# Kernel optimization log

Measured on AMD Instinct MI355X. Metric: run time of the kernel, lower is better.

## Reference

```python
import jax, jax.numpy as jnp
import numpy as np


def setup_inputs() -> dict:
    key = jax.random.key(0)
    k1, k2 = jax.random.split(key)
    B, D, T_ENC, T_DEC = 16, 256, 512, 2048
    x = jax.random.normal(k1, (B, D, T_ENC), dtype=jnp.float32)
    path = jax.random.uniform(k2, (B, T_ENC, T_DEC), dtype=jnp.float32)
    return {"x": x, "path": path}


def reference(x, path):
    # Batched matmul: [B, D, T_enc] @ [B, T_enc, T_dec] -> [B, D, T_dec]
    return jnp.einsum('bde,bet->bdt', x, path)
```

## Files before the change

kernel.cpp:

```cpp
#include <hip/hip_runtime.h>
#include <hip/hip_bf16.h>

#define NB 16
#define ND 256
#define NK 512
#define NT 2048

#define BM 128
#define BN 128
#define BK 32
#define RSA 40
#define RSB 36

typedef __attribute__((ext_vector_type(8))) short short8;
typedef __attribute__((ext_vector_type(4))) float f32x4;

union S8U { short8 v; uint2 u[2]; };
union BF2U { __hip_bfloat162 h; unsigned int u; };

__device__ inline unsigned int pack2bf(float a, float b) {
    BF2U c; c.h = __float22bfloat162_rn(make_float2(a, b));
    return c.u;
}

__global__ __launch_bounds__(256, 2)
void bmm_bf16_mfma(const float* __restrict__ x, const float* __restrict__ path,
                   float* __restrict__ out) {
    const int n0 = blockIdx.x * BN;
    const int m0 = blockIdx.y * BM;
    const int b  = blockIdx.z;
    const int t    = threadIdx.x;
    const int lane = t & 63;
    const int wv   = t >> 6;
    const int wr   = (wv >> 1) * 64;
    const int wc   = (wv & 1) * 64;
    const int q    = lane >> 4;
    const int lm   = lane & 15;

    __shared__ unsigned short As[BM * RSA];
    __shared__ unsigned short Bs[BN * RSB];

    const float* xg = x    + ((size_t)b * ND + m0) * NK;
    const float* pg = path + (size_t)b * NK * NT + n0;

    f32x4 acc[4][4];
#pragma unroll
    for (int i = 0; i < 4; ++i)
#pragma unroll
        for (int j = 0; j < 4; ++j)
            acc[i][j] = (f32x4){0.f, 0.f, 0.f, 0.f};

    for (int k0 = 0; k0 < NK; k0 += BK) {
#pragma unroll
        for (int i = 0; i < 4; ++i) {
            int f   = t + i * 256;
            int row = f >> 3;
            int c4  = f & 7;
            float4 v = *reinterpret_cast<const float4*>(xg + (size_t)row * NK + k0 + c4 * 4);
            uint2 p;
            p.x = pack2bf(v.x, v.y);
            p.y = pack2bf(v.z, v.w);
            *reinterpret_cast<uint2*>(&As[row * RSA + c4 * 4]) = p;
        }
#pragma unroll
        for (int i = 0; i < 4; ++i) {
            int p   = wv * 4 + i;
            int kr4 = p >> 1;
            int ng  = p & 1;
            int n   = ng * 64 + lane;
            const float* src = pg + (size_t)(k0 + kr4 * 4) * NT + n;
            float f0 = src[0 * NT];
            float f1 = src[1 * NT];
            float f2 = src[2 * NT];
            float f3 = src[3 * NT];
            uint2 pk;
            pk.x = pack2bf(f0, f1);
            pk.y = pack2bf(f2, f3);
            *reinterpret_cast<uint2*>(&Bs[n * RSB + kr4 * 4]) = pk;
        }
        __syncthreads();

        short8 af[4];
        short8 bfr[4];
#pragma unroll
        for (int mt = 0; mt < 4; ++mt) {
            int row = wr + mt * 16 + lm;
            af[mt] = *reinterpret_cast<const short8*>(&As[row * RSA + q * 8]);
        }
#pragma unroll
        for (int nt = 0; nt < 4; ++nt) {
            int n = wc + nt * 16 + lm;
            S8U s;
            s.u[0] = *reinterpret_cast<const uint2*>(&Bs[n * RSB + q * 8]);
            s.u[1] = *reinterpret_cast<const uint2*>(&Bs[n * RSB + q * 8 + 4]);
            bfr[nt] = s.v;
        }
#pragma unroll
        for (int mt = 0; mt < 4; ++mt)
#pragma unroll
            for (int nt = 0; nt < 4; ++nt)
                acc[mt][nt] = __builtin_amdgcn_mfma_f32_16x16x32_bf16(
                    af[mt], bfr[nt], acc[mt][nt], 0, 0, 0);

        __syncthreads();
    }

    float* og = out + ((size_t)b * ND + m0 + wr) * NT + n0 + wc;
#pragma unroll
    for (int mt = 0; mt < 4; ++mt) {
#pragma unroll
        for (int r = 0; r < 4; ++r) {
            int row = mt * 16 + q * 4 + r;
#pragma unroll
            for (int nt = 0; nt < 4; ++nt) {
                int col = nt * 16 + lm;
                og[(size_t)row * NT + col] = acc[mt][nt][r];
            }
        }
    }
}

extern "C" void kernel_launch(void* const* d_in, const int* in_sizes, int n_in,
                              void* d_out, int out_size, void* d_ws, size_t ws_size,
                              hipStream_t stream) {
    const float* x    = (const float*)d_in[0];
    const float* path = (const float*)d_in[1];
    float* out        = (float*)d_out;
    dim3 grid(NT / BN, ND / BM, NB);
    dim3 block(256);
    bmm_bf16_mfma<<<grid, block, 0, stream>>>(x, path, out);
}
```

Before: 120.4 us.

## Double-buffer LDS tiles with register prefetch and shrink N tile to 64

Adds register prefetch of the next K tile's global data while MFMAs run on the current LDS buffer, then writes it into a second LDS buffer, leaving one barrier per iteration. Halves BN to 64, which doubles the grid and raises the launch-bounds occupancy hint to 4 blocks per CU, to increase parallelism and latency hiding. The trade-off is that each wave does half as many MFMAs per loaded A fragment, so arithmetic intensity drops and the x tile is reloaded twice as often. The path loads now read 8 consecutive k rows per lane.

```diff
diff --git a/kernel.cpp b/kernel.cpp
--- a/kernel.cpp
+++ b/kernel.cpp
@@ -7,10 +7,11 @@
 #define NT 2048
 
 #define BM 128
-#define BN 128
+#define BN 64
 #define BK 32
 #define RSA 40
 #define RSB 36
+#define KITERS (NK / BK)
 
 typedef __attribute__((ext_vector_type(8))) short short8;
 typedef __attribute__((ext_vector_type(4))) float f32x4;
@@ -23,7 +24,7 @@
     return c.u;
 }
 
-__global__ __launch_bounds__(256, 2)
+__global__ __launch_bounds__(256, 4)
 void bmm_bf16_mfma(const float* __restrict__ x, const float* __restrict__ path,
                    float* __restrict__ out) {
     const int n0 = blockIdx.x * BN;
@@ -33,75 +34,91 @@
     const int lane = t & 63;
     const int wv   = t >> 6;
     const int wr   = (wv >> 1) * 64;
-    const int wc   = (wv & 1) * 64;
+    const int wc   = (wv & 1) * 32;
     const int q    = lane >> 4;
     const int lm   = lane & 15;
 
-    __shared__ unsigned short As[BM * RSA];
-    __shared__ unsigned short Bs[BN * RSB];
+    __shared__ unsigned short As[2][BM * RSA];
+    __shared__ unsigned short Bs[2][BN * RSB];
 
     const float* xg = x    + ((size_t)b * ND + m0) * NK;
     const float* pg = path + (size_t)b * NK * NT + n0;
 
-    f32x4 acc[4][4];
+    f32x4 acc[4][2];
 #pragma unroll
     for (int i = 0; i < 4; ++i)
 #pragma unroll
-        for (int j = 0; j < 4; ++j)
+        for (int j = 0; j < 2; ++j)
             acc[i][j] = (f32x4){0.f, 0.f, 0.f, 0.f};
 
-    for (int k0 = 0; k0 < NK; k0 += BK) {
-#pragma unroll
-        for (int i = 0; i < 4; ++i) {
-            int f   = t + i * 256;
-            int row = f >> 3;
-            int c4  = f & 7;
-            float4 v = *reinterpret_cast<const float4*>(xg + (size_t)row * NK + k0 + c4 * 4);
-            uint2 p;
-            p.x = pack2bf(v.x, v.y);
-            p.y = pack2bf(v.z, v.w);
-            *reinterpret_cast<uint2*>(&As[row * RSA + c4 * 4]) = p;
-        }
-#pragma unroll
-        for (int i = 0; i < 4; ++i) {
-            int p   = wv * 4 + i;
-            int kr4 = p >> 1;
-            int ng  = p & 1;
-            int n   = ng * 64 + lane;
-            const float* src = pg + (size_t)(k0 + kr4 * 4) * NT + n;
-            float f0 = src[0 * NT];
-            float f1 = src[1 * NT];
-            float f2 = src[2 * NT];
-            float f3 = src[3 * NT];
-            uint2 pk;
-            pk.x = pack2bf(f0, f1);
-            pk.y = pack2bf(f2, f3);
-            *reinterpret_cast<uint2*>(&Bs[n * RSB + kr4 * 4]) = pk;
-        }
-        __syncthreads();
+    float4 aReg[4];
+    float  bReg[8];
+
+#define LOAD_TILE(k0)                                                         \
+    {                                                                         \
+        _Pragma("unroll")                                                     \
+        for (int i = 0; i < 4; ++i) {                                         \
+            int f = t + i * 256;                                              \
+            int row = f >> 3, c4 = f & 7;                                     \
+            aReg[i] = *reinterpret_cast<const float4*>(                       \
+                xg + (size_t)row * NK + (k0) + c4 * 4);                       \
+        }                                                                     \
+        _Pragma("unroll")                                                     \
+        for (int j = 0; j < 8; ++j)                                           \
+            bReg[j] = pg[(size_t)((k0) + wv * 8 + j) * NT + lane];            \
+    }
+
+#define STORE_TILE(buf)                                                       \
+    {                                                                         \
+        _Pragma("unroll")                                                     \
+        for (int i = 0; i < 4; ++i) {                                         \
+            int f = t + i * 256;                                              \
+            int row = f >> 3, c4 = f & 7;                                     \
+            uint2 p;                                                          \
+            p.x = pack2bf(aReg[i].x, aReg[i].y);                              \
+            p.y = pack2bf(aReg[i].z, aReg[i].w);                              \
+            *reinterpret_cast<uint2*>(&As[buf][row * RSA + c4 * 4]) = p;      \
+        }                                                                     \
+        uint2 pk0, pk1;                                                       \
+        pk0.x = pack2bf(bReg[0], bReg[1]);                                    \
+        pk0.y = pack2bf(bReg[2], bReg[3]);                                    \
+        pk1.x = pack2bf(bReg[4], bReg[5]);                                    \
+        pk1.y = pack2bf(bReg[6], bReg[7]);                                    \
+        *reinterpret_cast<uint2*>(&Bs[buf][lane * RSB + wv * 8]) = pk0;       \
+        *reinterpret_cast<uint2*>(&Bs[buf][lane * RSB + wv * 8 + 4]) = pk1;   \
+    }
+
+    LOAD_TILE(0)
+    STORE_TILE(0)
+    __syncthreads();
+
+    for (int it = 0; it < KITERS; ++it) {
+        const int cur = it & 1;
+        if (it + 1 < KITERS) LOAD_TILE((it + 1) * BK)
 
         short8 af[4];
-        short8 bfr[4];
+        short8 bfr[2];
 #pragma unroll
         for (int mt = 0; mt < 4; ++mt) {
             int row = wr + mt * 16 + lm;
-            af[mt] = *reinterpret_cast<const short8*>(&As[row * RSA + q * 8]);
+            af[mt] = *reinterpret_cast<const short8*>(&As[cur][row * RSA + q * 8]);
         }
 #pragma unroll
-        for (int nt = 0; nt < 4; ++nt) {
+        for (int nt = 0; nt < 2; ++nt) {
             int n = wc + nt * 16 + lm;
             S8U s;
-            s.u[0] = *reinterpret_cast<const uint2*>(&Bs[n * RSB + q * 8]);
-            s.u[1] = *reinterpret_cast<const uint2*>(&Bs[n * RSB + q * 8 + 4]);
+            s.u[0] = *reinterpret_cast<const uint2*>(&Bs[cur][n * RSB + q * 8]);
+            s.u[1] = *reinterpret_cast<const uint2*>(&Bs[cur][n * RSB + q * 8 + 4]);
             bfr[nt] = s.v;
         }
 #pragma unroll
         for (int mt = 0; mt < 4; ++mt)
 #pragma unroll
-            for (int nt = 0; nt < 4; ++nt)
+            for (int nt = 0; nt < 2; ++nt)
                 acc[mt][nt] = __builtin_amdgcn_mfma_f32_16x16x32_bf16(
                     af[mt], bfr[nt], acc[mt][nt], 0, 0, 0);
 
+        if (it + 1 < KITERS) STORE_TILE(1 - cur)
         __syncthreads();
     }
 
@@ -112,7 +129,7 @@
         for (int r = 0; r < 4; ++r) {
             int row = mt * 16 + q * 4 + r;
 #pragma unroll
-            for (int nt = 0; nt < 4; ++nt) {
+            for (int nt = 0; nt < 2; ++nt) {
                 int col = nt * 16 + lm;
                 og[(size_t)row * NT + col] = acc[mt][nt][r];
             }
```

Result: slower. 130.8 us (+8.6%).

## Load MFMA fragments directly from global memory, dropping LDS staging

Applied to the files above, without the earlier changes.

Removes the shared-memory tiles and both barriers per k-step. Each wave now loads its A and B operand fragments straight from global memory, converts them to bf16 in registers and feeds the MFMAs. This avoids LDS writes, reads and synchronisation, at the cost of redundant global or cache loads across waves. It also uses narrowly coalesced strided scalar loads for the B operand.

```diff
diff --git a/kernel.cpp b/kernel.cpp
--- a/kernel.cpp
+++ b/kernel.cpp
@@ -5,17 +5,12 @@
 #define ND 256
 #define NK 512
 #define NT 2048
-
-#define BM 128
-#define BN 128
 #define BK 32
-#define RSA 40
-#define RSB 36
 
 typedef __attribute__((ext_vector_type(8))) short short8;
 typedef __attribute__((ext_vector_type(4))) float f32x4;
 
-union S8U { short8 v; uint2 u[2]; };
+union S8U { short8 v; unsigned int u[4]; };
 union BF2U { __hip_bfloat162 h; unsigned int u; };
 
 __device__ inline unsigned int pack2bf(float a, float b) {
@@ -24,24 +19,26 @@
 }
 
 __global__ __launch_bounds__(256, 2)
-void bmm_bf16_mfma(const float* __restrict__ x, const float* __restrict__ path,
-                   float* __restrict__ out) {
-    const int n0 = blockIdx.x * BN;
-    const int m0 = blockIdx.y * BM;
+void bmm_direct(const float* __restrict__ x, const float* __restrict__ path,
+                float* __restrict__ out) {
+    const int n0 = blockIdx.x * 128;
+    const int m0 = blockIdx.y * 128;
     const int b  = blockIdx.z;
-    const int t    = threadIdx.x;
-    const int lane = t & 63;
-    const int wv   = t >> 6;
-    const int wr   = (wv >> 1) * 64;
-    const int wc   = (wv & 1) * 64;
+    const int lane = threadIdx.x & 63;
+    const int wv   = threadIdx.x >> 6;
+    const int wm   = (wv >> 1) * 64;
+    const int wn   = (wv & 1) * 64;
     const int q    = lane >> 4;
     const int lm   = lane & 15;
 
-    __shared__ unsigned short As[BM * RSA];
-    __shared__ unsigned short Bs[BN * RSB];
-
-    const float* xg = x    + ((size_t)b * ND + m0) * NK;
-    const float* pg = path + (size_t)b * NK * NT + n0;
+    const float* ag[4];
+#pragma unroll
+    for (int mt = 0; mt < 4; ++mt)
+        ag[mt] = x + ((size_t)b * ND + (m0 + wm + mt * 16 + lm)) * NK + q * 8;
+    const float* bg[4];
+#pragma unroll
+    for (int nt = 0; nt < 4; ++nt)
+        bg[nt] = path + ((size_t)b * NK + q * 8) * NT + (n0 + wn + nt * 16 + lm);
 
     f32x4 acc[4][4];
 #pragma unroll
@@ -50,51 +47,41 @@
         for (int j = 0; j < 4; ++j)
             acc[i][j] = (f32x4){0.f, 0.f, 0.f, 0.f};
 
-    for (int k0 = 0; k0 < NK; k0 += BK) {
-#pragma unroll
-        for (int i = 0; i < 4; ++i) {
-            int f   = t + i * 256;
-            int row = f >> 3;
-            int c4  = f & 7;
-            float4 v = *reinterpret_cast<const float4*>(xg + (size_t)row * NK + k0 + c4 * 4);
-            uint2 p;
-            p.x = pack2bf(v.x, v.y);
-            p.y = pack2bf(v.z, v.w);
-            *reinterpret_cast<uint2*>(&As[row * RSA + c4 * 4]) = p;
-        }
-#pragma unroll
-        for (int i = 0; i < 4; ++i) {
-            int p   = wv * 4 + i;
-            int kr4 = p >> 1;
-            int ng  = p & 1;
-            int n   = ng * 64 + lane;
-            const float* src = pg + (size_t)(k0 + kr4 * 4) * NT + n;
-            float f0 = src[0 * NT];
-            float f1 = src[1 * NT];
-            float f2 = src[2 * NT];
-            float f3 = src[3 * NT];
-            uint2 pk;
-            pk.x = pack2bf(f0, f1);
-            pk.y = pack2bf(f2, f3);
-            *reinterpret_cast<uint2*>(&Bs[n * RSB + kr4 * 4]) = pk;
-        }
-        __syncthreads();
-
-        short8 af[4];
-        short8 bfr[4];
+#pragma unroll 1
+    for (int kt = 0; kt < NK / BK; ++kt) {
+        float4 a0[4], a1[4];
 #pragma unroll
         for (int mt = 0; mt < 4; ++mt) {
-            int row = wr + mt * 16 + lm;
-            af[mt] = *reinterpret_cast<const short8*>(&As[row * RSA + q * 8]);
+            a0[mt] = *reinterpret_cast<const float4*>(ag[mt]);
+            a1[mt] = *reinterpret_cast<const float4*>(ag[mt] + 4);
+        }
+        float bv[4][8];
+#pragma unroll
+        for (int nt = 0; nt < 4; ++nt)
+#pragma unroll
+            for (int j = 0; j < 8; ++j)
+                bv[nt][j] = bg[nt][(size_t)j * NT];
+
+        short8 af[4], bfr[4];
+#pragma unroll
+        for (int mt = 0; mt < 4; ++mt) {
+            S8U s;
+            s.u[0] = pack2bf(a0[mt].x, a0[mt].y);
+            s.u[1] = pack2bf(a0[mt].z, a0[mt].w);
+            s.u[2] = pack2bf(a1[mt].x, a1[mt].y);
+            s.u[3] = pack2bf(a1[mt].z, a1[mt].w);
+            af[mt] = s.v;
         }
 #pragma unroll
         for (int nt = 0; nt < 4; ++nt) {
-            int n = wc + nt * 16 + lm;
             S8U s;
-            s.u[0] = *reinterpret_cast<const uint2*>(&Bs[n * RSB + q * 8]);
-            s.u[1] = *reinterpret_cast<const uint2*>(&Bs[n * RSB + q * 8 + 4]);
+            s.u[0] = pack2bf(bv[nt][0], bv[nt][1]);
+            s.u[1] = pack2bf(bv[nt][2], bv[nt][3]);
+            s.u[2] = pack2bf(bv[nt][4], bv[nt][5]);
+            s.u[3] = pack2bf(bv[nt][6], bv[nt][7]);
             bfr[nt] = s.v;
         }
+
 #pragma unroll
         for (int mt = 0; mt < 4; ++mt)
 #pragma unroll
@@ -102,22 +89,22 @@
                 acc[mt][nt] = __builtin_amdgcn_mfma_f32_16x16x32_bf16(
                     af[mt], bfr[nt], acc[mt][nt], 0, 0, 0);
 
-        __syncthreads();
+#pragma unroll
+        for (int mt = 0; mt < 4; ++mt) ag[mt] += BK;
+#pragma unroll
+        for (int nt = 0; nt < 4; ++nt) bg[nt] += (size_t)BK * NT;
     }
 
-    float* og = out + ((size_t)b * ND + m0 + wr) * NT + n0 + wc;
+    float* og = out + ((size_t)b * ND + (m0 + wm)) * NT + n0 + wn;
 #pragma unroll
-    for (int mt = 0; mt < 4; ++mt) {
+    for (int mt = 0; mt < 4; ++mt)
 #pragma unroll
         for (int r = 0; r < 4; ++r) {
             int row = mt * 16 + q * 4 + r;
 #pragma unroll
-            for (int nt = 0; nt < 4; ++nt) {
-                int col = nt * 16 + lm;
-                og[(size_t)row * NT + col] = acc[mt][nt][r];
-            }
+            for (int nt = 0; nt < 4; ++nt)
+                og[(size_t)row * NT + nt * 16 + lm] = acc[mt][nt][r];
         }
-    }
 }
 
 extern "C" void kernel_launch(void* const* d_in, const int* in_sizes, int n_in,
@@ -126,7 +113,7 @@
     const float* x    = (const float*)d_in[0];
     const float* path = (const float*)d_in[1];
     float* out        = (float*)d_out;
-    dim3 grid(NT / BN, ND / BM, NB);
+    dim3 grid(NT / 128, ND / 128, NB);
     dim3 block(256);
-    bmm_bf16_mfma<<<grid, block, 0, stream>>>(x, path, out);
+    bmm_direct<<<grid, block, 0, stream>>>(x, path, out);
 }
```

Result: slower. 225.2 us (+87.0%).

## Stage full A slab in swizzled LDS and stream B from registers without barriers

Applied to the files above, without the earlier changes.

The kernel now loads the whole 64x512 slab of x into LDS once, as bf16 with an XOR swizzle, behind a single barrier. Each wave then reads its B fragments straight from global memory into registers, double-buffered across K steps, and converts them in registers, so the per-iteration LDS staging of B and both barriers disappear. The tile shrinks to 64x128 with each wave owning 32 columns, which doubles the grid and the number of times path is re-read from global memory. The 64 KB of LDS per block may limit occupancy, and the B loads (eight rows per lane) may be poorly coalesced.

```diff
diff --git a/kernel.cpp b/kernel.cpp
--- a/kernel.cpp
+++ b/kernel.cpp
@@ -5,17 +5,13 @@
 #define ND 256
 #define NK 512
 #define NT 2048
-
-#define BM 128
+#define BM 64
 #define BN 128
-#define BK 32
-#define RSA 40
-#define RSB 36
 
 typedef __attribute__((ext_vector_type(8))) short short8;
 typedef __attribute__((ext_vector_type(4))) float f32x4;
 
-union S8U { short8 v; uint2 u[2]; };
+union S8U { short8 v; unsigned int u[4]; };
 union BF2U { __hip_bfloat162 h; unsigned int u; };
 
 __device__ inline unsigned int pack2bf(float a, float b) {
@@ -24,100 +20,107 @@
 }
 
 __global__ __launch_bounds__(256, 2)
-void bmm_bf16_mfma(const float* __restrict__ x, const float* __restrict__ path,
-                   float* __restrict__ out) {
+void bmm_nobar(const float* __restrict__ x, const float* __restrict__ path,
+               float* __restrict__ out) {
     const int n0 = blockIdx.x * BN;
     const int m0 = blockIdx.y * BM;
     const int b  = blockIdx.z;
     const int t    = threadIdx.x;
     const int lane = t & 63;
     const int wv   = t >> 6;
-    const int wr   = (wv >> 1) * 64;
-    const int wc   = (wv & 1) * 64;
+    const int wn   = wv * 32;
     const int q    = lane >> 4;
     const int lm   = lane & 15;
 
-    __shared__ unsigned short As[BM * RSA];
-    __shared__ unsigned short Bs[BN * RSB];
+    __shared__ unsigned short As[BM * NK];
 
-    const float* xg = x    + ((size_t)b * ND + m0) * NK;
-    const float* pg = path + (size_t)b * NK * NT + n0;
+    const float* pgB = path + (size_t)b * NK * NT + n0 + wn;
 
-    f32x4 acc[4][4];
+    float bv0[2][8], bv1[2][8];
+#pragma unroll
+    for (int nt = 0; nt < 2; ++nt)
+#pragma unroll
+        for (int j = 0; j < 8; ++j)
+            bv0[nt][j] = pgB[(size_t)(q * 8 + j) * NT + nt * 16 + lm];
+
+    const float* xg = x + ((size_t)b * ND + m0) * NK;
+#pragma unroll
+    for (int i = 0; i < 32; ++i) {
+        int f   = t + i * 256;
+        int row = f >> 7, c4 = f & 127;
+        float4 v = *reinterpret_cast<const float4*>(xg + (size_t)row * NK + c4 * 4);
+        uint2 p;
+        p.x = pack2bf(v.x, v.y);
+        p.y = pack2bf(v.z, v.w);
+        int chunk = (c4 >> 1) ^ (row & 7);
+        *reinterpret_cast<uint2*>(&As[row * NK + chunk * 8 + (c4 & 1) * 4]) = p;
+    }
+    __syncthreads();
+
+    f32x4 acc[4][2];
 #pragma unroll
     for (int i = 0; i < 4; ++i)
 #pragma unroll
-        for (int j = 0; j < 4; ++j)
+        for (int j = 0; j < 2; ++j)
             acc[i][j] = (f32x4){0.f, 0.f, 0.f, 0.f};
 
-    for (int k0 = 0; k0 < NK; k0 += BK) {
-#pragma unroll
-        for (int i = 0; i < 4; ++i) {
-            int f   = t + i * 256;
-            int row = f >> 3;
-            int c4  = f & 7;
-            float4 v = *reinterpret_cast<const float4*>(xg + (size_t)row * NK + k0 + c4 * 4);
-            uint2 p;
-            p.x = pack2bf(v.x, v.y);
-            p.y = pack2bf(v.z, v.w);
-            *reinterpret_cast<uint2*>(&As[row * RSA + c4 * 4]) = p;
-        }
-#pragma unroll
-        for (int i = 0; i < 4; ++i) {
-            int p   = wv * 4 + i;
-            int kr4 = p >> 1;
-            int ng  = p & 1;
-            int n   = ng * 64 + lane;
-            const float* src = pg + (size_t)(k0 + kr4 * 4) * NT + n;
-            float f0 = src[0 * NT];
-            float f1 = src[1 * NT];
-            float f2 = src[2 * NT];
-            float f3 = src[3 * NT];
-            uint2 pk;
-            pk.x = pack2bf(f0, f1);
-            pk.y = pack2bf(f2, f3);
-            *reinterpret_cast<uint2*>(&Bs[n * RSB + kr4 * 4]) = pk;
-        }
-        __syncthreads();
-
-        short8 af[4];
-        short8 bfr[4];
-#pragma unroll
-        for (int mt = 0; mt < 4; ++mt) {
-            int row = wr + mt * 16 + lm;
-            af[mt] = *reinterpret_cast<const short8*>(&As[row * RSA + q * 8]);
-        }
-#pragma unroll
-        for (int nt = 0; nt < 4; ++nt) {
-            int n = wc + nt * 16 + lm;
-            S8U s;
-            s.u[0] = *reinterpret_cast<const uint2*>(&Bs[n * RSB + q * 8]);
-            s.u[1] = *reinterpret_cast<const uint2*>(&Bs[n * RSB + q * 8 + 4]);
-            bfr[nt] = s.v;
-        }
-#pragma unroll
-        for (int mt = 0; mt < 4; ++mt)
-#pragma unroll
-            for (int nt = 0; nt < 4; ++nt)
-                acc[mt][nt] = __builtin_amdgcn_mfma_f32_16x16x32_bf16(
-                    af[mt], bfr[nt], acc[mt][nt], 0, 0, 0);
-
-        __syncthreads();
+#define LOAD_B(dst, kt)                                                       \
+    {                                                                         \
+        const float* s_ = pgB + (size_t)((kt) * 32 + q * 8) * NT;             \
+        _Pragma("unroll")                                                     \
+        for (int nt = 0; nt < 2; ++nt)                                        \
+            _Pragma("unroll")                                                 \
+            for (int j = 0; j < 8; ++j)                                       \
+                dst[nt][j] = s_[(size_t)j * NT + nt * 16 + lm];               \
     }
 
-    float* og = out + ((size_t)b * ND + m0 + wr) * NT + n0 + wc;
+#define COMPUTE(kt, bv)                                                       \
+    {                                                                         \
+        short8 af[4], bfr[2];                                                 \
+        _Pragma("unroll")                                                     \
+        for (int mt = 0; mt < 4; ++mt) {                                      \
+            int row = mt * 16 + lm;                                           \
+            int chunk = ((kt) * 4 + q) ^ (lm & 7);                            \
+            af[mt] = *reinterpret_cast<const short8*>(&As[row * NK + chunk * 8]); \
+        }                                                                     \
+        _Pragma("unroll")                                                     \
+        for (int nt = 0; nt < 2; ++nt) {                                      \
+            S8U s;                                                            \
+            s.u[0] = pack2bf(bv[nt][0], bv[nt][1]);                           \
+            s.u[1] = pack2bf(bv[nt][2], bv[nt][3]);                           \
+            s.u[2] = pack2bf(bv[nt][4], bv[nt][5]);                           \
+            s.u[3] = pack2bf(bv[nt][6], bv[nt][7]);                           \
+            bfr[nt] = s.v;                                                    \
+        }                                                                     \
+        _Pragma("unroll")                                                     \
+        for (int mt = 0; mt < 4; ++mt)                                        \
+            _Pragma("unroll")                                                 \
+            for (int nt = 0; nt < 2; ++nt)                                    \
+                acc[mt][nt] = __builtin_amdgcn_mfma_f32_16x16x32_bf16(        \
+                    af[mt], bfr[nt], acc[mt][nt], 0, 0, 0);                   \
+    }
+
+#pragma unroll 1
+    for (int kt = 0; kt <= 12; kt += 2) {
+        LOAD_B(bv1, kt + 1)
+        COMPUTE(kt, bv0)
+        LOAD_B(bv0, kt + 2)
+        COMPUTE(kt + 1, bv1)
+    }
+    LOAD_B(bv1, 15)
+    COMPUTE(14, bv0)
+    COMPUTE(15, bv1)
+
+    float* og = out + ((size_t)b * ND + m0) * NT + n0 + wn;
 #pragma unroll
-    for (int mt = 0; mt < 4; ++mt) {
+    for (int mt = 0; mt < 4; ++mt)
 #pragma unroll
         for (int r = 0; r < 4; ++r) {
             int row = mt * 16 + q * 4 + r;
 #pragma unroll
-            for (int nt = 0; nt < 4; ++nt) {
-                int col = nt * 16 + lm;
-                og[(size_t)row * NT + col] = acc[mt][nt][r];
-            }
+            for (int nt = 0; nt < 2; ++nt)
+                og[(size_t)row * NT + nt * 16 + lm] = acc[mt][nt][r];
         }
-    }
 }
 
 extern "C" void kernel_launch(void* const* d_in, const int* in_sizes, int n_in,
@@ -128,5 +131,5 @@
     float* out        = (float*)d_out;
     dim3 grid(NT / BN, ND / BM, NB);
     dim3 block(256);
-    bmm_bf16_mfma<<<grid, block, 0, stream>>>(x, path, out);
+    bmm_nobar<<<grid, block, 0, stream>>>(x, path, out);
 }
```

After: 132.8 us. 1.1x slower.
